# Kernel optimization log

Measured on AMD Instinct MI355X. Metric: run time of the kernel, lower is better.

## Reference

```python
import jax, jax.numpy as jnp
import numpy as np

HEADS = 8
DIM_HEAD = 64
EPS = 1e-5  # nn.InstanceNorm1d default


def _inst_norm(t):
    # t: [b, h, n, d]; InstanceNorm1d(dim_head) on (b*h, n, d) input normalizes
    # over the last (L) axis per (instance, channel) = per (b, h, n) token.
    mu = jnp.mean(t, axis=-1, keepdims=True)
    var = jnp.var(t, axis=-1, keepdims=True)  # biased, matches torch eval-mode IN
    return (t - mu) / jnp.sqrt(var + EPS)


def setup_inputs() -> dict:
    key = jax.random.key(0)
    k1, k2, k3, k4 = jax.random.split(key, 4)
    b, n, dim = 4, 8192, 256
    inner = HEADS * DIM_HEAD  # 512
    x = jax.random.normal(k1, (b, n, dim), dtype=jnp.float32)
    w_qkv = jax.random.normal(k2, (dim, 3 * inner), dtype=jnp.float32) * (1.0 / DIM_HEAD)
    w_out = jax.random.normal(k3, (inner, dim), dtype=jnp.float32) * (dim ** -0.5)
    b_out = jax.random.normal(k4, (dim,), dtype=jnp.float32) * 0.01
    return {"x": x, "w_qkv": w_qkv, "w_out": w_out, "b_out": b_out}


def reference(x, w_qkv, w_out, b_out):
    b, n, dim = x.shape
    qkv = x @ w_qkv                                   # [b, n, 3*inner]
    q, k, v = jnp.split(qkv, 3, axis=-1)
    to_heads = lambda t: t.reshape(b, n, HEADS, DIM_HEAD).transpose(0, 2, 1, 3)  # b h n d
    q, k, v = to_heads(q), to_heads(k), to_heads(v)
    # Galerkin: instance-norm K and V
    k = _inst_norm(k)
    v = _inst_norm(v)
    # associative linear attention: (k^T v) then q @ dots, scaled by 1/n
    dots = jnp.einsum('bhnd,bhne->bhde', k, v)        # [b, h, d, d]
    out = jnp.einsum('bhnd,bhde->bhne', q, dots) * (1.0 / n)  # [b, h, n, d]
    out = out.transpose(0, 2, 1, 3).reshape(b, n, HEADS * DIM_HEAD)
    return out @ w_out + b_out                        # dropout p=0 (eval)
```

## Files before the change

### kernel.cpp

```cpp
#include <hip/hip_runtime.h>
#include <hip/hip_bf16.h>
#include <stdint.h>

#define HEADS 8
#define DHEAD 64
#define BATCH 4
#define SEQ   8192
#define DIM   256
#define INNER 512
#define QKVC  1536
#define ROWS  32768
#define EPS   1e-5f

typedef unsigned short u16;
typedef unsigned long long u64;
typedef __attribute__((ext_vector_type(8))) short bf16x8;
typedef __attribute__((ext_vector_type(4))) float f32x4;

#define AS1 __attribute__((address_space(1)))
#define AS3 __attribute__((address_space(3)))

__device__ __forceinline__ void async16(const void* g, void* l) {
  __builtin_amdgcn_global_load_lds((AS1 unsigned int*)g, (AS3 unsigned int*)l, 16, 0, 0);
}

__device__ __forceinline__ float bf2f(u16 u) {
  union { uint32_t i; float f; } v; v.i = ((uint32_t)u) << 16; return v.f;
}
__device__ __forceinline__ u16 f2bf(float f) {
  union { float f; uint32_t i; } v; v.f = f;
  uint32_t x = v.i;
  return (u16)((x + 0x7fffu + ((x >> 16) & 1u)) >> 16);
}

__global__ __launch_bounds__(256) void prep(const float* __restrict__ x,
                                            const float* __restrict__ w,
                                            u16* __restrict__ xb,
                                            u16* __restrict__ wqB,
                                            u16* __restrict__ wkvP,
                                            float* __restrict__ dots) {
  int bid = blockIdx.x;
  if (bid < 8192) {
    int i = (bid * 256 + threadIdx.x) * 4;
    float4 v = *(const float4*)(x + i);
    ushort4 o; o.x = f2bf(v.x); o.y = f2bf(v.y); o.z = f2bf(v.z); o.w = f2bf(v.w);
    *(ushort4*)(xb + i) = o;
  } else if (bid < 8704) {
    int id = (bid - 8192) * 256 + threadIdx.x;
    int k = id >> 9, j = id & 511;
    wqB[id] = f2bf(w[k * QKVC + j]);
  } else if (bid < 9728) {
    int id = (bid - 8704) * 256 + threadIdx.x;
    int j    = id & 7;
    int lane = (id >> 3) & 63;
    int frag = (id >> 9) & 63;
    int h    = id >> 15;
    int fn   = frag & 3;
    int half = (frag >> 2) & 1;
    int ks   = (frag >> 3) & 1;
    int kk   = frag >> 4;
    int col  = half * 64 + fn * 16 + (lane & 15);
    int kidx = kk * 64 + ks * 32 + (lane >> 4) * 8 + j;
    int oc   = (col < 64) ? (512 + h * 64 + col) : (1024 + h * 64 + (col - 64));
    wkvP[id] = f2bf(w[kidx * QKVC + oc]);
  } else {
    int i = ((bid - 9728) * 256 + threadIdx.x) * 4;
    float4 z; z.x = 0.f; z.y = 0.f; z.z = 0.f; z.w = 0.f;
    *(float4*)(dots + i) = z;
  }
}

__device__ __forceinline__ void gemm_tile(const u16* __restrict__ A, int lda,
                                          const u16* __restrict__ Bt, int ldb,
                                          int K, int row0, int col0,
                                          u16* sA, u16* sB, f32x4 acc[4][4]) {
  const int tid = threadIdx.x, lane = tid & 63, wave = tid >> 6;
  const int m = lane & 15, q = lane >> 4;
  const int mr = (wave >> 1) * 64, nc = (wave & 1) * 64;
  for (int kk = 0; kk < K; kk += 64) {
#pragma unroll
    for (int it = 0; it < 4; ++it) {
      int c = it * 256 + tid;
      int r = c >> 3, kc = (c ^ r) & 7;
      async16(A + (size_t)(row0 + r) * lda + kk + kc * 8, sA + (it * 256 + wave * 64) * 8);
      async16(Bt + (size_t)(col0 + r) * ldb + kk + kc * 8, sB + (it * 256 + wave * 64) * 8);
    }
    __syncthreads();
#pragma unroll
    for (int ks = 0; ks < 2; ++ks) {
      bf16x8 af[4], bfr[4];
#pragma unroll
      for (int f = 0; f < 4; ++f) {
        int ra = mr + f * 16 + m;
        int rb = nc + f * 16 + m;
        af[f]  = *(const bf16x8*)&sA[ra * 64 + (((ks * 4 + q) ^ (m & 7)) * 8)];
        bfr[f] = *(const bf16x8*)&sB[rb * 64 + (((ks * 4 + q) ^ (m & 7)) * 8)];
      }
#pragma unroll
      for (int fm = 0; fm < 4; ++fm)
#pragma unroll
        for (int fn = 0; fn < 4; ++fn)
          acc[fm][fn] = __builtin_amdgcn_mfma_f32_16x16x32_bf16(af[fm], bfr[fn], acc[fm][fn], 0, 0, 0);
    }
    __syncthreads();
  }
}

__global__ __launch_bounds__(256, 3) void gemm_kv_dots(const u16* __restrict__ A,
                                                       const u16* __restrict__ wkvP,
                                                       float* __restrict__ dots) {
  __shared__ alignas(16) u16 smem[17408];
  u16* sA  = smem;
  u16* knT = smem;
  u16* vnT = smem + 8704;

  const int tid = threadIdx.x, lane = tid & 63, wave = tid >> 6;
  const int m = lane & 15, q = lane >> 4;
  const int row0 = blockIdx.x * 128;
  const int h = blockIdx.y;
  const int half = wave & 1;
  const int rowbase = (wave >> 1) * 64;
  const u16* bp = wkvP + (size_t)h * 32768 + lane * 8;

  f32x4 acc[4][4];
#pragma unroll
  for (int i = 0; i < 4; ++i)
#pragma unroll
    for (int j = 0; j < 4; ++j) acc[i][j] = (f32x4){0.f, 0.f, 0.f, 0.f};

#pragma unroll
  for (int kk = 0; kk < 4; ++kk) {
    bf16x8 breg[2][4];
#pragma unroll
    for (int ks = 0; ks < 2; ++ks)
#pragma unroll
      for (int fn = 0; fn < 4; ++fn)
        breg[ks][fn] = *(const bf16x8*)(bp + (size_t)((((kk * 2 + ks) * 2 + half) * 4 + fn) * 512));
#pragma unroll
    for (int it = 0; it < 4; ++it) {
      int c = it * 256 + tid;
      int r = c >> 3, kc = (c ^ r) & 7;
      async16(A + (size_t)(row0 + r) * DIM + kk * 64 + kc * 8, sA + (it * 256 + wave * 64) * 8);
    }
    __syncthreads();
#pragma unroll
    for (int ks = 0; ks < 2; ++ks) {
      bf16x8 af[4];
#pragma unroll
      for (int f = 0; f < 4; ++f) {
        int r = rowbase + f * 16 + m;
        af[f] = *(const bf16x8*)&sA[r * 64 + (((ks * 4 + q) ^ (m & 7)) * 8)];
      }
#pragma unroll
      for (int fm = 0; fm < 4; ++fm)
#pragma unroll
        for (int fn = 0; fn < 4; ++fn)
          acc[fm][fn] = __builtin_amdgcn_mfma_f32_16x16x32_bf16(af[fm], breg[ks][fn], acc[fm][fn], 0, 0, 0);
    }
    __syncthreads();
  }

  u16* dst = half ? vnT : knT;
#pragma unroll
  for (int fm = 0; fm < 4; ++fm) {
    f32x4 s  = acc[fm][0] + acc[fm][1] + acc[fm][2] + acc[fm][3];
    f32x4 s2 = (f32x4){0.f, 0.f, 0.f, 0.f};
#pragma unroll
    for (int fn = 0; fn < 4; ++fn)
#pragma unroll
      for (int r = 0; r < 4; ++r) s2[r] = fmaf(acc[fm][fn][r], acc[fm][fn][r], s2[r]);
#pragma unroll
    for (int mask = 1; mask <= 8; mask <<= 1) {
#pragma unroll
      for (int r = 0; r < 4; ++r) {
        s[r]  += __shfl_xor(s[r],  mask, 64);
        s2[r] += __shfl_xor(s2[r], mask, 64);
      }
    }
    f32x4 mu, rs;
#pragma unroll
    for (int r = 0; r < 4; ++r) {
      mu[r] = s[r] * (1.f / 64.f);
      float var = s2[r] * (1.f / 64.f) - mu[r] * mu[r];
      rs[r] = rsqrtf(var + EPS);
    }
    const int tokb = rowbase + fm * 16 + q * 4;
#pragma unroll
    for (int fn = 0; fn < 4; ++fn) {
      int d = fn * 16 + m;
      u64 pk = 0;
#pragma unroll
      for (int r = 0; r < 4; ++r) {
        u16 hv = f2bf((acc[fm][fn][r] - mu[r]) * rs[r]);
        pk |= (u64)hv << (16 * r);
      }
      *(u64*)(dst + d * 136 + tokb) = pk;
    }
  }
  __syncthreads();

  f32x4 dacc[4];
#pragma unroll
  for (int f = 0; f < 4; ++f) dacc[f] = (f32x4){0.f, 0.f, 0.f, 0.f};
#pragma unroll
  for (int ks = 0; ks < 4; ++ks) {
    bf16x8 a = *(const bf16x8*)&knT[(wave * 16 + m) * 136 + ks * 32 + q * 8];
#pragma unroll
    for (int fn = 0; fn < 4; ++fn) {
      bf16x8 bb = *(const bf16x8*)&vnT[(fn * 16 + m) * 136 + ks * 32 + q * 8];
      dacc[fn] = __builtin_amdgcn_mfma_f32_16x16x32_bf16(a, bb, dacc[fn], 0, 0, 0);
    }
  }

  const int b = blockIdx.x >> 6;
  float* dbase = dots + (size_t)(b * 8 + h) * 4096;
#pragma unroll
  for (int fn = 0; fn < 4; ++fn) {
    int e = fn * 16 + m;
#pragma unroll
    for (int r = 0; r < 4; ++r) {
      int d = wave * 16 + q * 4 + r;
      atomicAdd(dbase + d * 64 + e, dacc[fn][r]);
    }
  }
}

__global__ __launch_bounds__(256) void make_M(const float* __restrict__ dots,
                                              const float* __restrict__ wout,
                                              u16* __restrict__ Mbt) {
  __shared__ float dl[8][64];
  const int bh = blockIdx.x, b = bh >> 3, h = bh & 7;
  const int jg = blockIdx.y;
  const int c = threadIdx.x;
  for (int i = threadIdx.x; i < 512; i += 256)
    ((float*)dl)[i] = dots[(size_t)bh * 4096 + jg * 512 + i];
  __syncthreads();
  float accv[8];
#pragma unroll
  for (int jj = 0; jj < 8; ++jj) accv[jj] = 0.f;
  for (int e = 0; e < 64; ++e) {
    float w = wout[(h * 64 + e) * DIM + c];
#pragma unroll
    for (int jj = 0; jj < 8; ++jj) accv[jj] = fmaf(dl[jj][e], w, accv[jj]);
  }
  const float inv_n = 1.0f / (float)SEQ;
  u16* outp = Mbt + ((size_t)(b * 256 + c)) * 512 + h * 64 + jg * 8;
#pragma unroll
  for (int jj = 0; jj < 8; ++jj) outp[jj] = f2bf(accv[jj] * inv_n);
}

__global__ __launch_bounds__(256) void make_G(const u16* __restrict__ Mbt,
                                              const u16* __restrict__ wqB,
                                              u16* __restrict__ Gt) {
  __shared__ alignas(16) u16 sA[128 * 64];
  __shared__ alignas(16) u16 sB[128 * 64];
  const int lane = threadIdx.x & 63, wave = threadIdx.x >> 6;
  const int row0 = blockIdx.x * 128, col0 = blockIdx.y * 128;
  const int b = blockIdx.z;
  f32x4 acc[4][4];
#pragma unroll
  for (int i = 0; i < 4; ++i)
#pragma unroll
    for (int j = 0; j < 4; ++j) acc[i][j] = (f32x4){0.f, 0.f, 0.f, 0.f};

  gemm_tile(Mbt + (size_t)b * 256 * 512, INNER, wqB, INNER, INNER, row0, col0, sA, sB, acc);

  u16* out = Gt + (size_t)b * 256 * 256;
  const int mr = (wave >> 1) * 64, nc = (wave & 1) * 64;
#pragma unroll
  for (int fm = 0; fm < 4; ++fm) {
    int rbase = row0 + mr + fm * 16 + (lane >> 4) * 4;
#pragma unroll
    for (int fn = 0; fn < 4; ++fn) {
      int col = col0 + nc + fn * 16 + (lane & 15);
#pragma unroll
      for (int r = 0; r < 4; ++r)
        out[(size_t)(rbase + r) * DIM + col] = f2bf(acc[fm][fn][r]);
    }
  }
}

__global__ __launch_bounds__(256) void gemm_out(const u16* __restrict__ A,
                                                const u16* __restrict__ Gt,
                                                const float* __restrict__ bias,
                                                float* __restrict__ out) {
  __shared__ alignas(16) u16 sA[128 * 64];
  __shared__ alignas(16) u16 sB[128 * 64];
  const int lane = threadIdx.x & 63, wave = threadIdx.x >> 6;
  const int row0 = blockIdx.x * 128, col0 = blockIdx.y * 128;
  const int b = blockIdx.x >> 6;
  const u16* Bt = Gt + (size_t)b * 256 * 256;
  f32x4 acc[4][4];
#pragma unroll
  for (int i = 0; i < 4; ++i)
#pragma unroll
    for (int j = 0; j < 4; ++j) acc[i][j] = (f32x4){0.f, 0.f, 0.f, 0.f};

  gemm_tile(A, DIM, Bt, DIM, DIM, row0, col0, sA, sB, acc);

  const int mr = (wave >> 1) * 64, nc = (wave & 1) * 64;
#pragma unroll
  for (int fm = 0; fm < 4; ++fm) {
    int rbase = row0 + mr + fm * 16 + (lane >> 4) * 4;
#pragma unroll
    for (int fn = 0; fn < 4; ++fn) {
      int col = col0 + nc + fn * 16 + (lane & 15);
      float bb = bias[col];
#pragma unroll
      for (int r = 0; r < 4; ++r)
        out[(size_t)(rbase + r) * DIM + col] = acc[fm][fn][r] + bb;
    }
  }
}

extern "C" void kernel_launch(void* const* d_in, const int* in_sizes, int n_in,
                              void* d_out, int out_size, void* d_ws, size_t ws_size,
                              hipStream_t stream) {
  const float* x     = (const float*)d_in[0];
  const float* w_qkv = (const float*)d_in[1];
  const float* w_out = (const float*)d_in[2];
  const float* b_out = (const float*)d_in[3];
  float* out = (float*)d_out;

  char* ws = (char*)d_ws;
  size_t off = 0;
  u16* xb    = (u16*)(ws + off); off += (size_t)ROWS * DIM * 2;
  u16* wqB   = (u16*)(ws + off); off += (size_t)DIM * INNER * 2;
  u16* wkvP  = (u16*)(ws + off); off += (size_t)HEADS * 128 * DIM * 2;
  float* dots = (float*)(ws + off); off += (size_t)32 * 64 * 64 * 4;
  u16* Mbt   = (u16*)(ws + off); off += (size_t)BATCH * 256 * 512 * 2;
  u16* Gt    = (u16*)(ws + off); off += (size_t)BATCH * 256 * 256 * 2;

  prep<<<9856, 256, 0, stream>>>(x, w_qkv, xb, wqB, wkvP, dots);
  gemm_kv_dots<<<dim3(ROWS / 128, HEADS), 256, 0, stream>>>(xb, wkvP, dots);
  make_M<<<dim3(32, 8), 256, 0, stream>>>(dots, w_out, Mbt);
  make_G<<<dim3(2, 2, BATCH), 256, 0, stream>>>(Mbt, wqB, Gt);
  gemm_out<<<dim3(ROWS / 128, 2), 256, 0, stream>>>(xb, Gt, b_out, out);
}
```

Baseline: 174.5 us.

## Replace atomic dots accumulation with per-block partials reduced in make_M

```diff
diff --git a/kernel.cpp b/kernel.cpp
--- a/kernel.cpp
+++ b/kernel.cpp
@@ -37,8 +37,7 @@
                                             const float* __restrict__ w,
                                             u16* __restrict__ xb,
                                             u16* __restrict__ wqB,
-                                            u16* __restrict__ wkvP,
-                                            float* __restrict__ dots) {
+                                            u16* __restrict__ wkvP) {
   int bid = blockIdx.x;
   if (bid < 8192) {
     int i = (bid * 256 + threadIdx.x) * 4;
@@ -49,7 +48,7 @@
     int id = (bid - 8192) * 256 + threadIdx.x;
     int k = id >> 9, j = id & 511;
     wqB[id] = f2bf(w[k * QKVC + j]);
-  } else if (bid < 9728) {
+  } else {
     int id = (bid - 8704) * 256 + threadIdx.x;
     int j    = id & 7;
     int lane = (id >> 3) & 63;
@@ -63,10 +62,6 @@
     int kidx = kk * 64 + ks * 32 + (lane >> 4) * 8 + j;
     int oc   = (col < 64) ? (512 + h * 64 + col) : (1024 + h * 64 + (col - 64));
     wkvP[id] = f2bf(w[kidx * QKVC + oc]);
-  } else {
-    int i = ((bid - 9728) * 256 + threadIdx.x) * 4;
-    float4 z; z.x = 0.f; z.y = 0.f; z.z = 0.f; z.w = 0.f;
-    *(float4*)(dots + i) = z;
   }
 }
 
@@ -108,7 +103,7 @@
 
 __global__ __launch_bounds__(256, 3) void gemm_kv_dots(const u16* __restrict__ A,
                                                        const u16* __restrict__ wkvP,
-                                                       float* __restrict__ dots) {
+                                                       float* __restrict__ pdots) {
   __shared__ alignas(16) u16 smem[17408];
   u16* sA  = smem;
   u16* knT = smem;
@@ -116,124 +111,134 @@
 
   const int tid = threadIdx.x, lane = tid & 63, wave = tid >> 6;
   const int m = lane & 15, q = lane >> 4;
-  const int row0 = blockIdx.x * 128;
   const int h = blockIdx.y;
   const int half = wave & 1;
   const int rowbase = (wave >> 1) * 64;
   const u16* bp = wkvP + (size_t)h * 32768 + lane * 8;
 
-  f32x4 acc[4][4];
-#pragma unroll
-  for (int i = 0; i < 4; ++i)
-#pragma unroll
-    for (int j = 0; j < 4; ++j) acc[i][j] = (f32x4){0.f, 0.f, 0.f, 0.f};
-
-#pragma unroll
-  for (int kk = 0; kk < 4; ++kk) {
-    bf16x8 breg[2][4];
-#pragma unroll
-    for (int ks = 0; ks < 2; ++ks)
+  f32x4 dacc[4];
+#pragma unroll
+  for (int f = 0; f < 4; ++f) dacc[f] = (f32x4){0.f, 0.f, 0.f, 0.f};
+
+  for (int t = 0; t < 4; ++t) {
+    const int row0 = (blockIdx.x * 4 + t) * 128;
+
+    f32x4 acc[4][4];
+#pragma unroll
+    for (int i = 0; i < 4; ++i)
+#pragma unroll
+      for (int j = 0; j < 4; ++j) acc[i][j] = (f32x4){0.f, 0.f, 0.f, 0.f};
+
+#pragma unroll
+    for (int kk = 0; kk < 4; ++kk) {
+      bf16x8 breg[2][4];
+#pragma unroll
+      for (int ks = 0; ks < 2; ++ks)
+#pragma unroll
+        for (int fn = 0; fn < 4; ++fn)
+          breg[ks][fn] = *(const bf16x8*)(bp + (size_t)((((kk * 2 + ks) * 2 + half) * 4 + fn) * 512));
+#pragma unroll
+      for (int it = 0; it < 4; ++it) {
+        int c = it * 256 + tid;
+        int r = c >> 3, kc = (c ^ r) & 7;
+        async16(A + (size_t)(row0 + r) * DIM + kk * 64 + kc * 8, sA + (it * 256 + wave * 64) * 8);
+      }
+      __syncthreads();
+#pragma unroll
+      for (int ks = 0; ks < 2; ++ks) {
+        bf16x8 af[4];
+#pragma unroll
+        for (int f = 0; f < 4; ++f) {
+          int r = rowbase + f * 16 + m;
+          af[f] = *(const bf16x8*)&sA[r * 64 + (((ks * 4 + q) ^ (m & 7)) * 8)];
+        }
+#pragma unroll
+        for (int fm = 0; fm < 4; ++fm)
+#pragma unroll
+          for (int fn = 0; fn < 4; ++fn)
+            acc[fm][fn] = __builtin_amdgcn_mfma_f32_16x16x32_bf16(af[fm], breg[ks][fn], acc[fm][fn], 0, 0, 0);
+      }
+      __syncthreads();
+    }
+
+    u16* dst = half ? vnT : knT;
+#pragma unroll
+    for (int fm = 0; fm < 4; ++fm) {
+      f32x4 s  = acc[fm][0] + acc[fm][1] + acc[fm][2] + acc[fm][3];
+      f32x4 s2 = (f32x4){0.f, 0.f, 0.f, 0.f};
 #pragma unroll
       for (int fn = 0; fn < 4; ++fn)
-        breg[ks][fn] = *(const bf16x8*)(bp + (size_t)((((kk * 2 + ks) * 2 + half) * 4 + fn) * 512));
-#pragma unroll
-    for (int it = 0; it < 4; ++it) {
-      int c = it * 256 + tid;
-      int r = c >> 3, kc = (c ^ r) & 7;
-      async16(A + (size_t)(row0 + r) * DIM + kk * 64 + kc * 8, sA + (it * 256 + wave * 64) * 8);
+#pragma unroll
+        for (int r = 0; r < 4; ++r) s2[r] = fmaf(acc[fm][fn][r], acc[fm][fn][r], s2[r]);
+#pragma unroll
+      for (int mask = 1; mask <= 8; mask <<= 1) {
+#pragma unroll
+        for (int r = 0; r < 4; ++r) {
+          s[r]  += __shfl_xor(s[r],  mask, 64);
+          s2[r] += __shfl_xor(s2[r], mask, 64);
+        }
+      }
+      f32x4 mu, rs;
+#pragma unroll
+      for (int r = 0; r < 4; ++r) {
+        mu[r] = s[r] * (1.f / 64.f);
+        float var = s2[r] * (1.f / 64.f) - mu[r] * mu[r];
+        rs[r] = rsqrtf(var + EPS);
+      }
+      const int tokb = rowbase + fm * 16 + q * 4;
+#pragma unroll
+      for (int fn = 0; fn < 4; ++fn) {
+        int d = fn * 16 + m;
+        u64 pk = 0;
+#pragma unroll
+        for (int r = 0; r < 4; ++r) {
+          u16 hv = f2bf((acc[fm][fn][r] - mu[r]) * rs[r]);
+          pk |= (u64)hv << (16 * r);
+        }
+        *(u64*)(dst + d * 136 + tokb) = pk;
+      }
     }
     __syncthreads();
-#pragma unroll
-    for (int ks = 0; ks < 2; ++ks) {
-      bf16x8 af[4];
-#pragma unroll
-      for (int f = 0; f < 4; ++f) {
-        int r = rowbase + f * 16 + m;
-        af[f] = *(const bf16x8*)&sA[r * 64 + (((ks * 4 + q) ^ (m & 7)) * 8)];
-      }
-#pragma unroll
-      for (int fm = 0; fm < 4; ++fm)
-#pragma unroll
-        for (int fn = 0; fn < 4; ++fn)
-          acc[fm][fn] = __builtin_amdgcn_mfma_f32_16x16x32_bf16(af[fm], breg[ks][fn], acc[fm][fn], 0, 0, 0);
+
+#pragma unroll
+    for (int ks = 0; ks < 4; ++ks) {
+      bf16x8 a = *(const bf16x8*)&knT[(wave * 16 + m) * 136 + ks * 32 + q * 8];
+#pragma unroll
+      for (int fn = 0; fn < 4; ++fn) {
+        bf16x8 bb = *(const bf16x8*)&vnT[(fn * 16 + m) * 136 + ks * 32 + q * 8];
+        dacc[fn] = __builtin_amdgcn_mfma_f32_16x16x32_bf16(a, bb, dacc[fn], 0, 0, 0);
+      }
     }
     __syncthreads();
   }
 
-  u16* dst = half ? vnT : knT;
-#pragma unroll
-  for (int fm = 0; fm < 4; ++fm) {
-    f32x4 s  = acc[fm][0] + acc[fm][1] + acc[fm][2] + acc[fm][3];
-    f32x4 s2 = (f32x4){0.f, 0.f, 0.f, 0.f};
-#pragma unroll
-    for (int fn = 0; fn < 4; ++fn)
-#pragma unroll
-      for (int r = 0; r < 4; ++r) s2[r] = fmaf(acc[fm][fn][r], acc[fm][fn][r], s2[r]);
-#pragma unroll
-    for (int mask = 1; mask <= 8; mask <<= 1) {
-#pragma unroll
-      for (int r = 0; r < 4; ++r) {
-        s[r]  += __shfl_xor(s[r],  mask, 64);
-        s2[r] += __shfl_xor(s2[r], mask, 64);
-      }
-    }
-    f32x4 mu, rs;
-#pragma unroll
-    for (int r = 0; r < 4; ++r) {
-      mu[r] = s[r] * (1.f / 64.f);
-      float var = s2[r] * (1.f / 64.f) - mu[r] * mu[r];
-      rs[r] = rsqrtf(var + EPS);
-    }
-    const int tokb = rowbase + fm * 16 + q * 4;
-#pragma unroll
-    for (int fn = 0; fn < 4; ++fn) {
-      int d = fn * 16 + m;
-      u64 pk = 0;
-#pragma unroll
-      for (int r = 0; r < 4; ++r) {
-        u16 hv = f2bf((acc[fm][fn][r] - mu[r]) * rs[r]);
-        pk |= (u64)hv << (16 * r);
-      }
-      *(u64*)(dst + d * 136 + tokb) = pk;
-    }
-  }
-  __syncthreads();
-
-  f32x4 dacc[4];
-#pragma unroll
-  for (int f = 0; f < 4; ++f) dacc[f] = (f32x4){0.f, 0.f, 0.f, 0.f};
-#pragma unroll
-  for (int ks = 0; ks < 4; ++ks) {
-    bf16x8 a = *(const bf16x8*)&knT[(wave * 16 + m) * 136 + ks * 32 + q * 8];
-#pragma unroll
-    for (int fn = 0; fn < 4; ++fn) {
-      bf16x8 bb = *(const bf16x8*)&vnT[(fn * 16 + m) * 136 + ks * 32 + q * 8];
-      dacc[fn] = __builtin_amdgcn_mfma_f32_16x16x32_bf16(a, bb, dacc[fn], 0, 0, 0);
-    }
-  }
-
-  const int b = blockIdx.x >> 6;
-  float* dbase = dots + (size_t)(b * 8 + h) * 4096;
+  const int b = blockIdx.x >> 4, p = blockIdx.x & 15;
+  float* pb = pdots + ((size_t)((b * 8 + h) * 16 + p)) * 4096;
 #pragma unroll
   for (int fn = 0; fn < 4; ++fn) {
     int e = fn * 16 + m;
 #pragma unroll
     for (int r = 0; r < 4; ++r) {
       int d = wave * 16 + q * 4 + r;
-      atomicAdd(dbase + d * 64 + e, dacc[fn][r]);
-    }
-  }
-}
-
-__global__ __launch_bounds__(256) void make_M(const float* __restrict__ dots,
+      pb[d * 64 + e] = dacc[fn][r];
+    }
+  }
+}
+
+__global__ __launch_bounds__(256) void make_M(const float* __restrict__ pdots,
                                               const float* __restrict__ wout,
                                               u16* __restrict__ Mbt) {
   __shared__ float dl[8][64];
   const int bh = blockIdx.x, b = bh >> 3, h = bh & 7;
   const int jg = blockIdx.y;
   const int c = threadIdx.x;
-  for (int i = threadIdx.x; i < 512; i += 256)
-    ((float*)dl)[i] = dots[(size_t)bh * 4096 + jg * 512 + i];
+  for (int i = threadIdx.x; i < 512; i += 256) {
+    const float* src = pdots + (size_t)bh * 16 * 4096 + jg * 512 + i;
+    float sum = 0.f;
+#pragma unroll
+    for (int p = 0; p < 16; ++p) sum += src[(size_t)p * 4096];
+    ((float*)dl)[i] = sum;
+  }
   __syncthreads();
   float accv[8];
 #pragma unroll
@@ -327,13 +332,13 @@
   u16* xb    = (u16*)(ws + off); off += (size_t)ROWS * DIM * 2;
   u16* wqB   = (u16*)(ws + off); off += (size_t)DIM * INNER * 2;
   u16* wkvP  = (u16*)(ws + off); off += (size_t)HEADS * 128 * DIM * 2;
-  float* dots = (float*)(ws + off); off += (size_t)32 * 64 * 64 * 4;
+  float* pdots = (float*)(ws + off); off += (size_t)32 * 16 * 4096 * 4;
   u16* Mbt   = (u16*)(ws + off); off += (size_t)BATCH * 256 * 512 * 2;
   u16* Gt    = (u16*)(ws + off); off += (size_t)BATCH * 256 * 256 * 2;
 
-  prep<<<9856, 256, 0, stream>>>(x, w_qkv, xb, wqB, wkvP, dots);
-  gemm_kv_dots<<<dim3(ROWS / 128, HEADS), 256, 0, stream>>>(xb, wkvP, dots);
-  make_M<<<dim3(32, 8), 256, 0, stream>>>(dots, w_out, Mbt);
+  prep<<<9728, 256, 0, stream>>>(x, w_qkv, xb, wqB, wkvP);
+  gemm_kv_dots<<<dim3(ROWS / 512, HEADS), 256, 0, stream>>>(xb, wkvP, pdots);
+  make_M<<<dim3(32, 8), 256, 0, stream>>>(pdots, w_out, Mbt);
   make_G<<<dim3(2, 2, BATCH), 256, 0, stream>>>(Mbt, wqB, Gt);
   gemm_out<<<dim3(ROWS / 128, 2), 256, 0, stream>>>(xb, Gt, b_out, out);
 }
```

Result: slower. 185.4 us (+6.2%).
